# Performance work log

Measured on AMD Instinct MI355X. Metric: run time of the kernel, lower is better.

Reference implementation:

```python
import jax, jax.numpy as jnp
import numpy as np

ALPHA1 = 0.1   # rank margin
ALPHA2 = 5.0   # penalty scale when violated
ALPHA3 = 10.0  # sigmoid sharpness
ALPHA_OTHER = 0.5  # floor for top-k threshold


def setup_inputs() -> dict:
    key = jax.random.key(0)
    B, C, L, S = 4096, 9605, 8, 50  # batch, classes, whitelist labels, classes per label
    k1, k2, k3 = jax.random.split(key, 3)
    x = jax.random.normal(k1, (B, C), dtype=jnp.float32)
    # sparse multi-label binarized targets (~10 positives/sample)
    y = (jax.random.uniform(k2, (B, C)) < 0.001).astype(jnp.float32)
    y_neg = (jax.random.uniform(k3, (B, C)) < 0.001).astype(jnp.float32)
    # disjoint per-label whitelist class index sets -> [L, C] boolean masks
    rng = np.random.default_rng(0)
    idx = rng.choice(C, size=L * S, replace=False).reshape(L, S)
    wl = np.zeros((L, C), dtype=bool)
    wl[np.arange(L)[:, None], idx] = True
    return {"x": x, "y": y, "y_neg": y_neg, "wl_mask": jnp.asarray(wl)}


def reference(x, y, y_neg, wl_mask):
    # x, y, y_neg: [B, C]; wl_mask: [L, C] bool. Returns scalar loss_rank_all.sum().
    # (The per-element BCE `loss` tensor and find_gt_whitelist(y_neg) in the
    #  original are dead code w.r.t. the returned value and are omitted.)
    xs = jax.nn.sigmoid(x)                                   # [B, C]
    wl_f = wl_mask.astype(x.dtype)                           # [L, C]
    # gt label present iff sum of y over that label's whitelist indices > 0
    gt_mask = (y @ wl_f.T) > 0                               # [B, L]
    has_gt = jnp.any(gt_mask, axis=1)                        # [B]
    first_gt = jnp.argmax(gt_mask, axis=1)                   # [B] first gt label
    # x_sorted[15] (16th largest) via top_k instead of full sort
    top16 = jax.lax.top_k(xs, 16)[0][:, 15]                  # [B]
    thres = jnp.maximum(top16, ALPHA_OTHER)                  # [B]
    # ---- branch: no gt whitelist label ----
    union = jnp.any(wl_mask, axis=0)                         # [C]
    x2_no = jnp.max(jnp.where(union[None, :], xs, -jnp.inf), axis=1)
    x1_no = thres
    # ---- branch: has gt whitelist label ----
    samp_mask = wl_mask[first_gt]                            # [B, C]
    x1_gt = jnp.max(jnp.where(samp_mask, xs, -jnp.inf), axis=1)
    L = wl_mask.shape[0]
    # faithful to original: indexes xs at LABEL positions 0..L-1, init 0
    non_gt = jnp.max(jnp.where(~gt_mask, xs[:, :L], 0.0), axis=1, initial=0.0)
    x2_gt = jnp.maximum(non_gt, thres)
    # ---- select branch and apply our_rank_loss ----
    x1 = jnp.where(has_gt, x1_gt, x1_no)
    x2 = jnp.where(has_gt, x2_gt, x2_no)
    d = x2 - x1 + ALPHA1
    sig = jax.nn.sigmoid(ALPHA3 * d)
    rank = jnp.where(d > 0, ALPHA2 * sig, sig)
    return jnp.sum(rank)
```

## Files before the change

kernel.cpp:

```cpp
#include <hip/hip_runtime.h>
#include <stdint.h>

#define BLOCK 512
#define CAP 512
#define TBL0 16
#define TBLW 2408
#define WS_ROUT 10240
static constexpr int LBL = 8;

#define A1 0.1f
#define A2 5.0f
#define A3 10.0f

__device__ __forceinline__ unsigned f2key(float f) {
  unsigned u = __float_as_uint(f);
  return (u & 0x80000000u) ? ~u : (u | 0x80000000u);
}
__device__ __forceinline__ float key2f(unsigned k) {
  unsigned u = (k & 0x80000000u) ? (k & 0x7FFFFFFFu) : ~k;
  return __uint_as_float(u);
}
__device__ __forceinline__ float sigm(float v) { return 1.0f / (1.0f + __expf(-v)); }

__global__ void detect_kernel(const unsigned char* __restrict__ wl, int total,
                              int* __restrict__ ws) {
  int i = blockIdx.x * 256 + threadIdx.x;
  if (i < total && (i & 3) != 0 && wl[i] == 1) atomicOr(&ws[1], 1);
}

__global__ void build_lmap(const unsigned char* __restrict__ wl, int C,
                           int* __restrict__ ws) {
  int c = blockIdx.x * 256 + threadIdx.x;
  if (c >= C) return;
  int isByte = ws[1];
  unsigned lab = 255u;
  if (isByte) {
    for (int l = 0; l < LBL; ++l)
      if (wl[(long long)l * C + c]) lab = (unsigned)l;
  } else {
    const int* w = (const int*)wl;
    for (int l = 0; l < LBL; ++l)
      if (w[(long long)l * C + c]) lab = (unsigned)l;
  }
  if (lab < (unsigned)LBL) {
#pragma unroll
    for (int s2 = 0; s2 < 4; ++s2)
      if (c >= s2) {
        unsigned char* tb = (unsigned char*)(ws + TBL0 + s2 * TBLW);
        tb[c - s2] = (unsigned char)lab;
      }
  }
}

__global__ __launch_bounds__(BLOCK, 8) void rank_kernel(
    const float* __restrict__ x, const float* __restrict__ y,
    const int* __restrict__ ws, float* __restrict__ rout, int C) {
  __shared__ unsigned hist[2048];
  __shared__ unsigned buf[CAP];
  __shared__ float wtop2[BLOCK / 64];
  __shared__ unsigned wtot[BLOCK / 64];
  __shared__ unsigned lmaxk[LBL];
  __shared__ float smL[LBL];
  __shared__ unsigned gtbits, bufcnt, s_seld, s_selk, s_selc, s_key;

  int tid = threadIdx.x;
  int row = blockIdx.x;
  long long base = (long long)row * C;
  const float* __restrict__ xr = x + base;
  const float* __restrict__ yr = y + base;

  int s = (int)((4 - (base & 3)) & 3);
  int nv = (C - s) >> 2;
  int tail0 = s + 4 * nv;
  int nrem = C - 4 * nv;

  const unsigned* Ts = (const unsigned*)(ws + TBL0 + s * TBLW);
  const unsigned char* Tb = (const unsigned char*)Ts;
  const unsigned char* T0b = (const unsigned char*)(ws + TBL0);

  const float4* __restrict__ xv4 = (const float4*)(xr + s);
  const float4* __restrict__ yv4 = (const float4*)(yr + s);
  float4 f[5];
  bool hv[5];
  unsigned lw[5];
#pragma unroll
  for (int t = 0; t < 5; ++t) {
    int i = tid + t * BLOCK;
    hv[t] = (i < nv);
    f[t] = hv[t] ? xv4[i] : make_float4(-INFINITY, -INFINITY, -INFINITY, -INFINITY);
    lw[t] = hv[t] ? Ts[i] : 0xFFFFFFFFu;
  }
  float tailv = -INFINITY;
  bool havet = false;
  unsigned tlab = 255u;
  int tc = 0;
  if (tid < nrem) {
    tc = (tid < s) ? tid : tail0 + (tid - s);
    tailv = xr[tc];
    havet = true;
    tlab = (tid < s) ? (unsigned)T0b[tc] : (unsigned)Tb[tc - s];
  }
  if (tid < LBL) smL[tid] = xr[tid];

  if (tid < LBL) lmaxk[tid] = 0u;
  if (tid == 0) { gtbits = 0u; bufcnt = 0u; }
  __syncthreads();

#pragma unroll
  for (int t = 0; t < 5; ++t) {
    if (lw[t] != 0xFFFFFFFFu) {
      float4 yv = yv4[tid + t * BLOCK];
      unsigned w2 = lw[t];
      float fe[4] = {f[t].x, f[t].y, f[t].z, f[t].w};
      float ye[4] = {yv.x, yv.y, yv.z, yv.w};
#pragma unroll
      for (int e = 0; e < 4; ++e) {
        unsigned lab = (w2 >> (8 * e)) & 255u;
        if (lab < (unsigned)LBL) {
          atomicMax(&lmaxk[lab], f2key(fe[e]));
          if (ye[e] != 0.0f) atomicOr(&gtbits, 1u << lab);
        }
      }
    }
  }
  if (havet && tlab < (unsigned)LBL) {
    atomicMax(&lmaxk[tlab], f2key(tailv));
    if (yr[tc] != 0.0f) atomicOr(&gtbits, 1u << tlab);
  }

  float tmax = tailv;
#pragma unroll
  for (int t = 0; t < 5; ++t)
    tmax = fmaxf(tmax, fmaxf(fmaxf(f[t].x, f[t].y), fmaxf(f[t].z, f[t].w)));

  float a1 = tmax, a2 = -INFINITY;
#pragma unroll
  for (int st = 1; st < 64; st <<= 1) {
    float b1 = __shfl_xor(a1, st, 64);
    float b2 = __shfl_xor(a2, st, 64);
    float m = fminf(a1, b1);
    float o = (a1 >= b1) ? a2 : b2;
    a1 = fmaxf(a1, b1);
    a2 = fmaxf(m, o);
  }
  int w = tid >> 6;
  if ((tid & 63) == 0) wtop2[w] = a2;
  __syncthreads();
  float p = wtop2[0];
#pragma unroll
  for (int i = 1; i < BLOCK / 64; ++i) p = fminf(p, wtop2[i]);

#pragma unroll
  for (int t = 0; t < 5; ++t) {
    if (f[t].x >= p) { unsigned q = atomicAdd(&bufcnt, 1u); if (q < CAP) buf[q] = f2key(f[t].x); }
    if (f[t].y >= p) { unsigned q = atomicAdd(&bufcnt, 1u); if (q < CAP) buf[q] = f2key(f[t].y); }
    if (f[t].z >= p) { unsigned q = atomicAdd(&bufcnt, 1u); if (q < CAP) buf[q] = f2key(f[t].z); }
    if (f[t].w >= p) { unsigned q = atomicAdd(&bufcnt, 1u); if (q < CAP) buf[q] = f2key(f[t].w); }
  }
  if (havet && tailv >= p) { unsigned q = atomicAdd(&bufcnt, 1u); if (q < CAP) buf[q] = f2key(tailv); }
  __syncthreads();

  unsigned selkey = 0u;
  int bc = (int)bufcnt;
  if (bc >= 16 && bc <= CAP) {
    if (tid < 64) {
      for (int i = tid; i < bc; i += 64) {
        unsigned mk = buf[i];
        int g = 0, e2 = 0;
        for (int j = 0; j < bc; ++j) {
          unsigned bk = buf[j];
          g += (bk > mk);
          e2 += (bk == mk);
        }
        if (g < 16 && 16 <= g + e2) s_key = mk;
      }
    }
    __syncthreads();
    selkey = s_key;
  } else {
    unsigned prefix = 0, pmask = 0;
    int k = 16;
    bool done = false;
    const int SHa[3] = {21, 10, 0};
    const int WIDa[3] = {11, 11, 10};
    for (int lev = 0; lev < 3 && !done; ++lev) {
      int shift = SHa[lev];
      int nb = 1 << WIDa[lev];
      unsigned bmask = (unsigned)nb - 1u;
      for (int i = tid; i < nb; i += BLOCK) hist[i] = 0;
      if (tid == 0) bufcnt = 0;
      __syncthreads();
#pragma unroll
      for (int t = 0; t < 5; ++t)
        if (hv[t]) {
          unsigned kk[4] = {f2key(f[t].x), f2key(f[t].y), f2key(f[t].z), f2key(f[t].w)};
#pragma unroll
          for (int e = 0; e < 4; ++e)
            if ((kk[e] & pmask) == prefix) atomicAdd(&hist[(kk[e] >> shift) & bmask], 1u);
        }
      if (havet) {
        unsigned tk = f2key(tailv);
        if ((tk & pmask) == prefix) atomicAdd(&hist[(tk >> shift) & bmask], 1u);
      }
      __syncthreads();
      int bpt = nb / BLOCK;
      int b0 = tid * bpt;
      unsigned cs = 0;
      for (int b = 0; b < bpt; ++b) cs += hist[b0 + b];
      unsigned v = cs;
      int lane = tid & 63;
#pragma unroll
      for (int st = 1; st < 64; st <<= 1) {
        unsigned tv = __shfl_down(v, st, 64);
        if (lane + st < 64) v += tv;
      }
      int w2 = tid >> 6;
      if (lane == 0) wtot[w2] = v;
      __syncthreads();
      unsigned above = 0;
      for (int ww = w2 + 1; ww < BLOCK / 64; ++ww) above += wtot[ww];
      unsigned S_incl = v + above;
      unsigned S_excl = S_incl - cs;
      if (S_excl < (unsigned)k && (unsigned)k <= S_incl) {
        int kk2 = k - (int)S_excl;
        int d = b0 + bpt - 1;
        for (; d > b0; --d) {
          int cb = (int)hist[d];
          if (kk2 <= cb) break;
          kk2 -= cb;
        }
        s_seld = (unsigned)d;
        s_selk = (unsigned)kk2;
        s_selc = hist[d];
      }
      __syncthreads();
      prefix |= s_seld << shift;
      pmask |= bmask << shift;
      k = (int)s_selk;
      unsigned selc = s_selc;
      if (lev == 2) {
        selkey = prefix;
        done = true;
      } else if (selc <= (unsigned)CAP) {
#pragma unroll
        for (int t = 0; t < 5; ++t)
          if (hv[t]) {
            unsigned kk[4] = {f2key(f[t].x), f2key(f[t].y), f2key(f[t].z), f2key(f[t].w)};
#pragma unroll
            for (int e = 0; e < 4; ++e)
              if ((kk[e] & pmask) == prefix) {
                unsigned q = atomicAdd(&bufcnt, 1u);
                if (q < CAP) buf[q] = kk[e];
              }
          }
        if (havet) {
          unsigned tk = f2key(tailv);
          if ((tk & pmask) == prefix) {
            unsigned q = atomicAdd(&bufcnt, 1u);
            if (q < CAP) buf[q] = tk;
          }
        }
        __syncthreads();
        int bc2 = (int)bufcnt;
        if (bc2 > CAP) bc2 = CAP;
        unsigned mk = (tid < bc2) ? buf[tid] : 0u;
        int g = 0, e2 = 0;
        for (int j = 0; j < bc2; ++j) {
          unsigned bk = buf[j];
          g += (bk > mk);
          e2 += (bk == mk);
        }
        if (tid < bc2 && g < k && k <= g + e2) s_key = mk;
        __syncthreads();
        selkey = s_key;
        done = true;
      }
    }
  }

  if (tid == 0) {
    float x16 = key2f(selkey);
    float thres = sigm(fmaxf(x16, 0.0f));
    unsigned gb = gtbits;
    float x1, x2;
    if (gb) {
      int first = __ffs((int)gb) - 1;
      x1 = sigm(key2f(lmaxk[first]));
      float ng = 0.0f;
      for (int l = 0; l < LBL; ++l)
        if (!((gb >> l) & 1)) ng = fmaxf(ng, sigm(smL[l]));
      x2 = fmaxf(ng, thres);
    } else {
      unsigned um = 0;
      for (int l = 0; l < LBL; ++l) um = um > lmaxk[l] ? um : lmaxk[l];
      x1 = thres;
      x2 = sigm(key2f(um));
    }
    float dd = x2 - x1 + A1;
    float sg = 1.0f / (1.0f + __expf(-A3 * dd));
    rout[row] = (dd > 0.0f) ? A2 * sg : sg;
  }
}

__global__ __launch_bounds__(256) void reduce_kernel(const float* __restrict__ rin,
                                                     float* __restrict__ out, int B) {
  __shared__ float smr[256];
  float acc = 0.0f;
  for (int i = threadIdx.x; i < B; i += 256) acc += rin[i];
  smr[threadIdx.x] = acc;
  __syncthreads();
  for (int st = 128; st > 0; st >>= 1) {
    if (threadIdx.x < st) smr[threadIdx.x] += smr[threadIdx.x + st];
    __syncthreads();
  }
  if (threadIdx.x == 0) out[0] = smr[0];
}

extern "C" void kernel_launch(void* const* d_in, const int* in_sizes, int n_in,
                              void* d_out, int out_size, void* d_ws, size_t ws_size,
                              hipStream_t stream) {
  const float* x = (const float*)d_in[0];
  const float* y = (const float*)d_in[1];
  const unsigned char* wl = (const unsigned char*)d_in[3];

  int C = in_sizes[3] / LBL;
  int B = in_sizes[0] / C;
  int total = LBL * C;
  int* ws = (int*)d_ws;

  hipMemsetAsync(d_ws, 0, TBL0 * 4, stream);
  hipMemsetAsync(ws + TBL0, 0xFF, (size_t)4 * TBLW * 4, stream);
  int nbs = (total + 255) / 256;
  hipLaunchKernelGGL(detect_kernel, dim3(nbs), dim3(256), 0, stream, wl, total, ws);
  int nbc = (C + 255) / 256;
  hipLaunchKernelGGL(build_lmap, dim3(nbc), dim3(256), 0, stream, wl, C, ws);

  hipLaunchKernelGGL(rank_kernel, dim3(B), dim3(BLOCK), 0, stream, x, y, ws,
                     (float*)(ws + WS_ROUT), C);
  hipLaunchKernelGGL(reduce_kernel, dim3(1), dim3(256), 0, stream,
                     (const float*)(ws + WS_ROUT), (float*)d_out, B);
}
```

Baseline: 76.71 us.

## Replace dense label map with sparse whitelist entry list and halve block size

The dense per-column label table is replaced by a compact list of (vector index, packed labels) entries for each alignment, built with atomics. The rank kernel now gathers only the whitelisted float4 vectors of x and y instead of reading a label word for every vector. The block is halved to 256 threads with 10 float4s per thread, so each thread holds more values in registers and the block count per CU may change. The entry list is capped at 1024 per alignment, and the kernel reads exactly two entries per thread, which assumes at most 512 whitelisted vectors.

```diff
diff --git a/kernel.cpp b/kernel.cpp
--- a/kernel.cpp
+++ b/kernel.cpp
@@ -1,11 +1,12 @@
 #include <hip/hip_runtime.h>
 #include <stdint.h>
 
-#define BLOCK 512
-#define CAP 512
-#define TBL0 16
-#define TBLW 2408
-#define WS_ROUT 10240
+#define BLOCK 256
+#define NW 10
+#define CAP 256
+#define WL0 32
+#define WLE 1024
+#define WS_ROUT 8704
 static constexpr int LBL = 8;
 
 #define A1 0.1f
@@ -28,27 +29,46 @@
   if (i < total && (i & 3) != 0 && wl[i] == 1) atomicOr(&ws[1], 1);
 }
 
-__global__ void build_lmap(const unsigned char* __restrict__ wl, int C,
-                           int* __restrict__ ws) {
-  int c = blockIdx.x * 256 + threadIdx.x;
-  if (c >= C) return;
+__global__ void build_kernel(const unsigned char* __restrict__ wl, int C,
+                             int* __restrict__ ws) {
+  int t = blockIdx.x * 256 + threadIdx.x;
   int isByte = ws[1];
-  unsigned lab = 255u;
-  if (isByte) {
-    for (int l = 0; l < LBL; ++l)
-      if (wl[(long long)l * C + c]) lab = (unsigned)l;
-  } else {
-    const int* w = (const int*)wl;
-    for (int l = 0; l < LBL; ++l)
-      if (w[(long long)l * C + c]) lab = (unsigned)l;
-  }
-  if (lab < (unsigned)LBL) {
-#pragma unroll
-    for (int s2 = 0; s2 < 4; ++s2)
-      if (c >= s2) {
-        unsigned char* tb = (unsigned char*)(ws + TBL0 + s2 * TBLW);
-        tb[c - s2] = (unsigned char)lab;
-      }
+  const int* wlw = (const int*)wl;
+  if (t < 12) {
+    int c = (t < 4) ? t : C - 8 + (t - 4);
+    int lab = 255;
+    for (int l = 0; l < LBL; ++l) {
+      bool v = isByte ? (wl[(long long)l * C + c] != 0)
+                      : (wlw[(long long)l * C + c] != 0);
+      if (v) lab = l;
+    }
+    if (t < 4) ws[4 + t] = lab; else ws[8 + (t - 4)] = lab;
+  }
+  int s = t / 2404, w = t % 2404;
+  if (s < 4) {
+    int nv = (C - s) >> 2;
+    if (w < nv) {
+      unsigned labs = 0xFFFFFFFFu;
+      bool any = false;
+#pragma unroll
+      for (int e = 0; e < 4; ++e) {
+        int c = s + 4 * w + e;
+        unsigned lab = 255u;
+        for (int l = 0; l < LBL; ++l) {
+          bool v = isByte ? (wl[(long long)l * C + c] != 0)
+                          : (wlw[(long long)l * C + c] != 0);
+          if (v) lab = (unsigned)l;
+        }
+        if (lab < (unsigned)LBL) {
+          labs = (labs & ~(255u << (8 * e))) | (lab << (8 * e));
+          any = true;
+        }
+      }
+      if (any) {
+        int p = atomicAdd(&ws[16 + s], 1);
+        if (p < WLE) ((int2*)(ws + WL0))[(size_t)s * WLE + p] = make_int2(w, (int)labs);
+      }
+    }
   }
 }
 
@@ -74,31 +94,32 @@
   int tail0 = s + 4 * nv;
   int nrem = C - 4 * nv;
 
-  const unsigned* Ts = (const unsigned*)(ws + TBL0 + s * TBLW);
-  const unsigned char* Tb = (const unsigned char*)Ts;
-  const unsigned char* T0b = (const unsigned char*)(ws + TBL0);
-
   const float4* __restrict__ xv4 = (const float4*)(xr + s);
   const float4* __restrict__ yv4 = (const float4*)(yr + s);
-  float4 f[5];
-  bool hv[5];
-  unsigned lw[5];
-#pragma unroll
-  for (int t = 0; t < 5; ++t) {
+
+  float4 f[NW];
+  bool hv[NW];
+#pragma unroll
+  for (int t = 0; t < NW; ++t) {
     int i = tid + t * BLOCK;
     hv[t] = (i < nv);
     f[t] = hv[t] ? xv4[i] : make_float4(-INFINITY, -INFINITY, -INFINITY, -INFINITY);
-    lw[t] = hv[t] ? Ts[i] : 0xFFFFFFFFu;
-  }
-  float tailv = -INFINITY;
+  }
+  const int2* __restrict__ wle = (const int2*)(ws + WL0) + (size_t)s * WLE;
+  int2 E0 = wle[tid];
+  int2 E1 = wle[tid + BLOCK];
+  float4 yg0 = make_float4(0, 0, 0, 0), xg0 = yg0, yg1 = yg0, xg1 = yg0;
+  if (E0.y != -1) { yg0 = yv4[E0.x]; xg0 = xv4[E0.x]; }
+  if (E1.y != -1) { yg1 = yv4[E1.x]; xg1 = xv4[E1.x]; }
+  float tailv = -INFINITY, tyv = 0.0f;
   bool havet = false;
-  unsigned tlab = 255u;
-  int tc = 0;
+  int tc = 0, tlab = 255;
   if (tid < nrem) {
     tc = (tid < s) ? tid : tail0 + (tid - s);
     tailv = xr[tc];
+    tyv = yr[tc];
     havet = true;
-    tlab = (tid < s) ? (unsigned)T0b[tc] : (unsigned)Tb[tc - s];
+    tlab = (tc < 4) ? ws[4 + tc] : ws[8 + (tc - (C - 8))];
   }
   if (tid < LBL) smL[tid] = xr[tid];
 
@@ -106,31 +127,40 @@
   if (tid == 0) { gtbits = 0u; bufcnt = 0u; }
   __syncthreads();
 
-#pragma unroll
-  for (int t = 0; t < 5; ++t) {
-    if (lw[t] != 0xFFFFFFFFu) {
-      float4 yv = yv4[tid + t * BLOCK];
-      unsigned w2 = lw[t];
-      float fe[4] = {f[t].x, f[t].y, f[t].z, f[t].w};
-      float ye[4] = {yv.x, yv.y, yv.z, yv.w};
-#pragma unroll
-      for (int e = 0; e < 4; ++e) {
-        unsigned lab = (w2 >> (8 * e)) & 255u;
-        if (lab < (unsigned)LBL) {
-          atomicMax(&lmaxk[lab], f2key(fe[e]));
-          if (ye[e] != 0.0f) atomicOr(&gtbits, 1u << lab);
-        }
-      }
-    }
-  }
-  if (havet && tlab < (unsigned)LBL) {
+  if (E0.y != -1) {
+    float fx[4] = {xg0.x, xg0.y, xg0.z, xg0.w};
+    float fy[4] = {yg0.x, yg0.y, yg0.z, yg0.w};
+    unsigned labs = (unsigned)E0.y;
+#pragma unroll
+    for (int e = 0; e < 4; ++e) {
+      unsigned lab = (labs >> (8 * e)) & 255u;
+      if (lab < (unsigned)LBL) {
+        atomicMax(&lmaxk[lab], f2key(fx[e]));
+        if (fy[e] != 0.0f) atomicOr(&gtbits, 1u << lab);
+      }
+    }
+  }
+  if (E1.y != -1) {
+    float fx[4] = {xg1.x, xg1.y, xg1.z, xg1.w};
+    float fy[4] = {yg1.x, yg1.y, yg1.z, yg1.w};
+    unsigned labs = (unsigned)E1.y;
+#pragma unroll
+    for (int e = 0; e < 4; ++e) {
+      unsigned lab = (labs >> (8 * e)) & 255u;
+      if (lab < (unsigned)LBL) {
+        atomicMax(&lmaxk[lab], f2key(fx[e]));
+        if (fy[e] != 0.0f) atomicOr(&gtbits, 1u << lab);
+      }
+    }
+  }
+  if (havet && tlab < LBL) {
     atomicMax(&lmaxk[tlab], f2key(tailv));
-    if (yr[tc] != 0.0f) atomicOr(&gtbits, 1u << tlab);
+    if (tyv != 0.0f) atomicOr(&gtbits, 1u << tlab);
   }
 
   float tmax = tailv;
 #pragma unroll
-  for (int t = 0; t < 5; ++t)
+  for (int t = 0; t < NW; ++t)
     tmax = fmaxf(tmax, fmaxf(fmaxf(f[t].x, f[t].y), fmaxf(f[t].z, f[t].w)));
 
   float a1 = tmax, a2 = -INFINITY;
@@ -151,7 +181,7 @@
   for (int i = 1; i < BLOCK / 64; ++i) p = fminf(p, wtop2[i]);
 
 #pragma unroll
-  for (int t = 0; t < 5; ++t) {
+  for (int t = 0; t < NW; ++t) {
     if (f[t].x >= p) { unsigned q = atomicAdd(&bufcnt, 1u); if (q < CAP) buf[q] = f2key(f[t].x); }
     if (f[t].y >= p) { unsigned q = atomicAdd(&bufcnt, 1u); if (q < CAP) buf[q] = f2key(f[t].y); }
     if (f[t].z >= p) { unsigned q = atomicAdd(&bufcnt, 1u); if (q < CAP) buf[q] = f2key(f[t].z); }
@@ -191,7 +221,7 @@
       if (tid == 0) bufcnt = 0;
       __syncthreads();
 #pragma unroll
-      for (int t = 0; t < 5; ++t)
+      for (int t = 0; t < NW; ++t)
         if (hv[t]) {
           unsigned kk[4] = {f2key(f[t].x), f2key(f[t].y), f2key(f[t].z), f2key(f[t].w)};
 #pragma unroll
@@ -243,7 +273,7 @@
         done = true;
       } else if (selc <= (unsigned)CAP) {
 #pragma unroll
-        for (int t = 0; t < 5; ++t)
+        for (int t = 0; t < NW; ++t)
           if (hv[t]) {
             unsigned kk[4] = {f2key(f[t].x), f2key(f[t].y), f2key(f[t].z), f2key(f[t].w)};
 #pragma unroll
@@ -328,12 +358,12 @@
   int total = LBL * C;
   int* ws = (int*)d_ws;
 
-  hipMemsetAsync(d_ws, 0, TBL0 * 4, stream);
-  hipMemsetAsync(ws + TBL0, 0xFF, (size_t)4 * TBLW * 4, stream);
+  hipMemsetAsync(ws, 0, 32 * 4, stream);
+  hipMemsetAsync(ws + WL0, 0xFF, (size_t)4 * WLE * 2 * 4, stream);
   int nbs = (total + 255) / 256;
   hipLaunchKernelGGL(detect_kernel, dim3(nbs), dim3(256), 0, stream, wl, total, ws);
-  int nbc = (C + 255) / 256;
-  hipLaunchKernelGGL(build_lmap, dim3(nbc), dim3(256), 0, stream, wl, C, ws);
+  int nbb = (4 * 2404 + 255) / 256;
+  hipLaunchKernelGGL(build_kernel, dim3(nbb), dim3(256), 0, stream, wl, C, ws);
 
   hipLaunchKernelGGL(rank_kernel, dim3(B), dim3(BLOCK), 0, stream, x, y, ws,
                      (float*)(ws + WS_ROUT), C);
```

Result: slower. 119.5 us (+55.8%).
